# Performance work log

Measured on AMD Instinct MI355X. Metric: run time of the kernel, lower is better.

## Reference

```python
import jax, jax.numpy as jnp
import numpy as np

N_NODES = 50000
N_EDGES = 800000
HID = 256
HEADS = 4
HEAD_C = HID // HEADS  # 64
IN_CH = 16
OUT_CH = 4
NEG_SLOPE = 0.2  # PyG GATConv default LeakyReLU slope
LN_EPS = 1e-5


def setup_inputs() -> dict:
    key = jax.random.key(0)
    ks = jax.random.split(key, 12)
    s = 0.05
    return {
        "x": jax.random.normal(ks[0], (N_NODES, IN_CH), dtype=jnp.float32),
        "edge_index": jax.random.randint(ks[1], (2, N_EDGES), 0, N_NODES, dtype=jnp.int64),
        "w_in": jax.random.normal(ks[2], (IN_CH, HID), dtype=jnp.float32) * s,
        "b_in": jnp.zeros((HID,), dtype=jnp.float32),
        "w_gat": jax.random.normal(ks[3], (4, HID, HID), dtype=jnp.float32) * s,
        "att_src": jax.random.normal(ks[4], (4, HEADS, HEAD_C), dtype=jnp.float32) * s,
        "att_dst": jax.random.normal(ks[5], (4, HEADS, HEAD_C), dtype=jnp.float32) * s,
        "b_gat": jnp.zeros((4, HID), dtype=jnp.float32),
        "ln_scale": jnp.ones((4, HID), dtype=jnp.float32),
        "ln_bias": jnp.zeros((4, HID), dtype=jnp.float32),
        "w_out": jax.random.normal(ks[6], (HID, OUT_CH), dtype=jnp.float32) * s,
        "b_out": jnp.zeros((OUT_CH,), dtype=jnp.float32),
    }


def _gat_layer(x, src, dst, W, a_src, a_dst, bias, g, beta):
    """One GATConv(concat, heads=4) + LayerNorm + ELU. x:[N,HID]."""
    n = x.shape[0]
    h = (x @ W).reshape(n, HEADS, HEAD_C)                 # [N,H,C]
    a_s = jnp.einsum("nhc,hc->nh", h, a_src)              # [N,H]
    a_d = jnp.einsum("nhc,hc->nh", h, a_dst)              # [N,H]
    logits = jax.nn.leaky_relu(a_s[src] + a_d[dst], NEG_SLOPE)  # [E,H]
    # segment softmax over destination neighborhoods (self-loops ensure non-empty)
    m = jax.ops.segment_max(logits, dst, num_segments=n)
    e = jnp.exp(logits - m[dst])
    denom = jax.ops.segment_sum(e, dst, num_segments=n)
    alpha = e / (denom[dst] + 1e-16)                      # [E,H]
    msg = alpha[:, :, None] * h[src]                      # [E,H,C]
    out = jax.ops.segment_sum(msg, dst, num_segments=n).reshape(n, HID) + bias
    mu = out.mean(-1, keepdims=True)
    var = out.var(-1, keepdims=True)
    out = (out - mu) * jax.lax.rsqrt(var + LN_EPS) * g + beta
    return jax.nn.elu(out)


def reference(x, edge_index, w_in, b_in, w_gat, att_src, att_dst, b_gat,
              ln_scale, ln_bias, w_out, b_out):
    n = x.shape[0]
    # PyG GATConv adds self-loops by default
    loops = jnp.arange(n, dtype=edge_index.dtype)
    ei = jnp.concatenate([edge_index, jnp.stack([loops, loops])], axis=1)
    src, dst = ei[0], ei[1]

    x = x @ w_in + b_in                                   # input_proj
    h = x
    for l in (0, 1):
        h = _gat_layer(h, src, dst, w_gat[l], att_src[l], att_dst[l],
                       b_gat[l], ln_scale[l], ln_bias[l])
    x = x + h
    h = x
    for l in (2, 3):
        h = _gat_layer(h, src, dst, w_gat[l], att_src[l], att_dst[l],
                       b_gat[l], ln_scale[l], ln_bias[l])
    x = x + h
    return x @ w_out + b_out
```

## Files before the change

kernel.cpp:

```cpp
#include <hip/hip_runtime.h>
#include <math.h>

#define NN 50000
#define E0 800000
#define ET 850000
#define HID 256
#define INCH 16
#define MAXDEG 64

typedef _Float16 h8 __attribute__((ext_vector_type(8)));
typedef float f32x4 __attribute__((ext_vector_type(4)));

__global__ void scatter_pad_kernel(const int* __restrict__ ei, int* __restrict__ cursor,
                                   int* __restrict__ csr_pad) {
    int e = blockIdx.x * blockDim.x + threadIdx.x;
    if (e >= ET) return;
    int s, d;
    if (e < E0) { s = ei[e]; d = ei[E0 + e]; }
    else        { s = d = e - E0; }
    int pos = atomicAdd(&cursor[d], 1);
    if (pos < MAXDEG) csr_pad[(d << 6) + pos] = s;
}

__global__ __launch_bounds__(256) void wt_kernel(const float* __restrict__ w,
                                                 _Float16* __restrict__ wt) {
    int k = blockIdx.x, l = blockIdx.y, n = threadIdx.x;
    float v = w[((size_t)l * 256 + k) * 256 + n];
    wt[((size_t)l * 256 + n) * 256 + k] = (_Float16)v;
}

__global__ __launch_bounds__(256) void input_proj_kernel(
    const float* __restrict__ x, const float* __restrict__ w,
    const float* __restrict__ b, _Float16* __restrict__ outh) {
    int n = blockIdx.x, j = threadIdx.x;
    __shared__ float xs[INCH];
    if (j < INCH) xs[j] = x[n * INCH + j];
    __syncthreads();
    float acc = b[j];
#pragma unroll
    for (int k = 0; k < INCH; k++) acc += xs[k] * w[k * HID + j];
    outh[n * HID + j] = (_Float16)acc;
}

__global__ __launch_bounds__(512) void gemm_fused_kernel(
    const _Float16* __restrict__ A, const _Float16* __restrict__ BT,
    _Float16* __restrict__ H, const float* __restrict__ att_s,
    const float* __restrict__ att_d, float* __restrict__ AS, float* __restrict__ AD,
    int N) {
    int t = threadIdx.x;
    int wv = t >> 6, lane = t & 63;
    int rb = blockIdx.x * 128;
    int wr = (wv >> 2) * 64, wc = (wv & 3) * 64;
    int lm = lane & 15, lq = lane >> 4;
    f32x4 acc[4][4] = {};

    const _Float16* ap[4];
#pragma unroll
    for (int i = 0; i < 4; ++i) {
        int ra = rb + wr + i * 16 + lm;
        if (ra >= N) ra = N - 1;
        ap[i] = A + (size_t)ra * 256 + lq * 8;
    }
    const _Float16* bp[4];
#pragma unroll
    for (int j = 0; j < 4; ++j)
        bp[j] = BT + (size_t)(wc + j * 16 + lm) * 256 + lq * 8;

#pragma unroll 2
    for (int k0 = 0; k0 < 256; k0 += 32) {
        h8 af[4], bfr[4];
#pragma unroll
        for (int i = 0; i < 4; ++i) af[i] = *(const h8*)(ap[i] + k0);
#pragma unroll
        for (int j = 0; j < 4; ++j) bfr[j] = *(const h8*)(bp[j] + k0);
#pragma unroll
        for (int i = 0; i < 4; ++i)
#pragma unroll
            for (int j = 0; j < 4; ++j)
                acc[i][j] = __builtin_amdgcn_mfma_f32_16x16x32_f16(af[i], bfr[j], acc[i][j], 0, 0, 0);
    }

    int head = wv & 3;
    float sa[4], sd[4];
#pragma unroll
    for (int j = 0; j < 4; ++j) {
        sa[j] = att_s[head * 64 + j * 16 + lm];
        sd[j] = att_d[head * 64 + j * 16 + lm];
    }
#pragma unroll
    for (int i = 0; i < 4; ++i)
#pragma unroll
        for (int rr = 0; rr < 4; ++rr) {
            float vs = acc[i][0][rr] * sa[0] + acc[i][1][rr] * sa[1]
                     + acc[i][2][rr] * sa[2] + acc[i][3][rr] * sa[3];
            float vd = acc[i][0][rr] * sd[0] + acc[i][1][rr] * sd[1]
                     + acc[i][2][rr] * sd[2] + acc[i][3][rr] * sd[3];
#pragma unroll
            for (int o = 1; o <= 8; o <<= 1) {
                vs += __shfl_xor(vs, o, 64);
                vd += __shfl_xor(vd, o, 64);
            }
            int row = rb + wr + i * 16 + lq * 4 + rr;
            if (lm == 0 && row < N) {
                AS[row * 4 + head] = vs;
                AD[row * 4 + head] = vd;
            }
        }

#pragma unroll
    for (int i = 0; i < 4; ++i)
#pragma unroll
        for (int j = 0; j < 4; ++j) {
            int col = wc + j * 16 + lm;
#pragma unroll
            for (int rr = 0; rr < 4; ++rr) {
                int row = rb + wr + i * 16 + lq * 4 + rr;
                if (row < N) H[(size_t)row * 256 + col] = (_Float16)acc[i][j][rr];
            }
        }
}

__global__ __launch_bounds__(256) void agg_kernel(
    const _Float16* __restrict__ H, const float4* __restrict__ AS,
    const float4* __restrict__ AD,
    const int* __restrict__ cnt, const int* __restrict__ csr_pad,
    const float* __restrict__ bias, const float* __restrict__ g, const float* __restrict__ beta,
    const _Float16* __restrict__ res, _Float16* __restrict__ outh) {
    int t = threadIdx.x;
    int l32 = t & 31;
    int n = blockIdx.x * 8 + (t >> 5);
    int deg = cnt[n];
    if (deg > MAXDEG) deg = MAXDEG;
    int start = n << 6, end = start + deg;
    float4 adv = AD[n];
    int head = l32 >> 3;
    int c0 = l32 * 8;
    float advh = (head == 0) ? adv.x : (head == 1) ? adv.y : (head == 2) ? adv.z : adv.w;

    float acc[8] = {};
    float acc_e = 0.f;
#pragma unroll 4
    for (int i = start; i < end; ++i) {
        int s = csr_pad[i];
        const float* as = (const float*)&AS[s];
        float v = as[head] + advh;
        v = (v >= 0.f) ? v : 0.2f * v;
        float e = __expf(v);
        acc_e += e;
        h8 hv = *(const h8*)(H + (size_t)s * 256 + c0);
#pragma unroll
        for (int k = 0; k < 8; ++k) acc[k] += e * (float)hv[k];
    }
    float dinv = 1.f / (acc_e + 1e-16f);

    float val[8];
#pragma unroll
    for (int k = 0; k < 8; k += 4) {
        float4 bb = *(const float4*)(bias + c0 + k);
        val[k]     = acc[k]     * dinv + bb.x;
        val[k + 1] = acc[k + 1] * dinv + bb.y;
        val[k + 2] = acc[k + 2] * dinv + bb.z;
        val[k + 3] = acc[k + 3] * dinv + bb.w;
    }

    float s1 = 0.f, s2 = 0.f;
#pragma unroll
    for (int k = 0; k < 8; ++k) { s1 += val[k]; s2 += val[k] * val[k]; }
#pragma unroll
    for (int o = 16; o >= 1; o >>= 1) {
        s1 += __shfl_xor(s1, o, 64);
        s2 += __shfl_xor(s2, o, 64);
    }
    float mu = s1 * (1.f / 256.f);
    float var = s2 * (1.f / 256.f) - mu * mu;
    float rs = rsqrtf(var + 1e-5f);

    float y[8];
#pragma unroll
    for (int k = 0; k < 8; k += 4) {
        float4 g4 = *(const float4*)(g + c0 + k);
        float4 b4 = *(const float4*)(beta + c0 + k);
        y[k]     = (val[k]     - mu) * rs * g4.x + b4.x;
        y[k + 1] = (val[k + 1] - mu) * rs * g4.y + b4.y;
        y[k + 2] = (val[k + 2] - mu) * rs * g4.z + b4.z;
        y[k + 3] = (val[k + 3] - mu) * rs * g4.w + b4.w;
    }
#pragma unroll
    for (int k = 0; k < 8; ++k) y[k] = (y[k] > 0.f) ? y[k] : (__expf(y[k]) - 1.f);
    if (res) {
        h8 r0 = *(const h8*)(res + (size_t)n * 256 + c0);
#pragma unroll
        for (int k = 0; k < 8; ++k) y[k] += (float)r0[k];
    }
    h8 o0;
#pragma unroll
    for (int k = 0; k < 8; ++k) o0[k] = (_Float16)y[k];
    *(h8*)(outh + (size_t)n * 256 + c0) = o0;
}

__global__ __launch_bounds__(256) void out_proj_kernel(
    const _Float16* __restrict__ x, const float* __restrict__ w,
    const float* __restrict__ b, float* __restrict__ out, int n) {
    int tid = blockIdx.x * blockDim.x + threadIdx.x;
    int node = tid >> 6, lane = tid & 63;
    if (node >= n) return;
    const _Float16* xp = x + (size_t)node * HID + lane * 4;
    float x0 = (float)xp[0], x1 = (float)xp[1], x2 = (float)xp[2], x3 = (float)xp[3];
    const float4* wr = (const float4*)w;
    float4 w0 = wr[lane * 4 + 0];
    float4 w1 = wr[lane * 4 + 1];
    float4 w2 = wr[lane * 4 + 2];
    float4 w3 = wr[lane * 4 + 3];
    float o0 = x0 * w0.x + x1 * w1.x + x2 * w2.x + x3 * w3.x;
    float o1 = x0 * w0.y + x1 * w1.y + x2 * w2.y + x3 * w3.y;
    float o2 = x0 * w0.z + x1 * w1.z + x2 * w2.z + x3 * w3.z;
    float o3 = x0 * w0.w + x1 * w1.w + x2 * w2.w + x3 * w3.w;
#pragma unroll
    for (int o = 32; o >= 1; o >>= 1) {
        o0 += __shfl_down(o0, o, 64);
        o1 += __shfl_down(o1, o, 64);
        o2 += __shfl_down(o2, o, 64);
        o3 += __shfl_down(o3, o, 64);
    }
    if (lane == 0) {
        out[node * 4 + 0] = o0 + b[0];
        out[node * 4 + 1] = o1 + b[1];
        out[node * 4 + 2] = o2 + b[2];
        out[node * 4 + 3] = o3 + b[3];
    }
}

extern "C" void kernel_launch(void* const* d_in, const int* in_sizes, int n_in,
                              void* d_out, int out_size, void* d_ws, size_t ws_size,
                              hipStream_t stream) {
    const float* x       = (const float*)d_in[0];
    const int*   ei      = (const int*)  d_in[1];
    const float* w_in    = (const float*)d_in[2];
    const float* b_in    = (const float*)d_in[3];
    const float* w_gat   = (const float*)d_in[4];
    const float* att_src = (const float*)d_in[5];
    const float* att_dst = (const float*)d_in[6];
    const float* b_gat   = (const float*)d_in[7];
    const float* ln_g    = (const float*)d_in[8];
    const float* ln_b    = (const float*)d_in[9];
    const float* w_out   = (const float*)d_in[10];
    const float* b_out   = (const float*)d_in[11];
    float* out = (float*)d_out;

    char* ws = (char*)d_ws;
    size_t off = 0;
    auto alloc = [&](size_t bytes) {
        void* p = ws + off;
        off += (bytes + 255) & ~(size_t)255;
        return p;
    };
    _Float16*  Ph      = (_Float16*)alloc((size_t)NN * HID * 2);
    _Float16*  Ch      = (_Float16*)alloc((size_t)NN * HID * 2);
    _Float16*  Gh      = (_Float16*)alloc((size_t)NN * HID * 2);
    _Float16*  H       = (_Float16*)alloc((size_t)NN * HID * 2);
    _Float16*  WT      = (_Float16*)alloc((size_t)4 * HID * HID * 2);
    float*     ASAD    = (float*)alloc((size_t)NN * 8 * 4);
    int*       cursor  = (int*)alloc((size_t)NN * 4);
    int*       csr_pad = (int*)alloc((size_t)NN * MAXDEG * 4);

    float* AS = ASAD;
    float* AD = ASAD + (size_t)NN * 4;

    const int NB_EDGE = (ET + 255) / 256;
    const int NB_GEMM = (NN + 127) / 128;
    const int NB_AGG = NN / 8;

    hipMemsetAsync(cursor, 0, (size_t)NN * 4, stream);
    scatter_pad_kernel<<<NB_EDGE, 256, 0, stream>>>(ei, cursor, csr_pad);

    wt_kernel<<<dim3(256, 4), 256, 0, stream>>>(w_gat, WT);
    input_proj_kernel<<<NN, 256, 0, stream>>>(x, w_in, b_in, Ph);

    auto run_layer = [&](const _Float16* inh, int l, const _Float16* res, _Float16* outh) {
        gemm_fused_kernel<<<NB_GEMM, 512, 0, stream>>>(
            inh, WT + (size_t)l * HID * HID, H,
            att_src + l * 256, att_dst + l * 256, AS, AD, NN);
        agg_kernel<<<NB_AGG, 256, 0, stream>>>(
            H, (const float4*)AS, (const float4*)AD, cursor, csr_pad,
            b_gat + l * 256, ln_g + l * 256, ln_b + l * 256, res, outh);
    };

    run_layer(Ph, 0, nullptr, Gh);
    run_layer(Gh, 1, Ph,      Ch);
    run_layer(Ch, 2, nullptr, Gh);
    run_layer(Gh, 3, Ch,      Ph);

    out_proj_kernel<<<(NN * 64 + 255) / 256, 256, 0, stream>>>(Ph, w_out, b_out, out, NN);
}
```

Before: 616.1 us.

## Fuse all stages into one persistent cooperative kernel with grid syncs

```diff
diff --git a/kernel.cpp b/kernel.cpp
--- a/kernel.cpp
+++ b/kernel.cpp
@@ -1,5 +1,8 @@
 #include <hip/hip_runtime.h>
+#include <hip/hip_cooperative_groups.h>
 #include <math.h>
+
+namespace cg = cooperative_groups;
 
 #define NN 50000
 #define E0 800000
@@ -7,246 +10,268 @@
 #define HID 256
 #define INCH 16
 #define MAXDEG 64
-
+#define NT64 782
+#define NGRP (NN / 8)
+
+typedef _Float16 h4 __attribute__((ext_vector_type(4)));
 typedef _Float16 h8 __attribute__((ext_vector_type(8)));
 typedef float f32x4 __attribute__((ext_vector_type(4)));
 
-__global__ void scatter_pad_kernel(const int* __restrict__ ei, int* __restrict__ cursor,
-                                   int* __restrict__ csr_pad) {
-    int e = blockIdx.x * blockDim.x + threadIdx.x;
-    if (e >= ET) return;
-    int s, d;
-    if (e < E0) { s = ei[e]; d = ei[E0 + e]; }
-    else        { s = d = e - E0; }
-    int pos = atomicAdd(&cursor[d], 1);
-    if (pos < MAXDEG) csr_pad[(d << 6) + pos] = s;
-}
-
-__global__ __launch_bounds__(256) void wt_kernel(const float* __restrict__ w,
-                                                 _Float16* __restrict__ wt) {
-    int k = blockIdx.x, l = blockIdx.y, n = threadIdx.x;
-    float v = w[((size_t)l * 256 + k) * 256 + n];
-    wt[((size_t)l * 256 + n) * 256 + k] = (_Float16)v;
-}
-
-__global__ __launch_bounds__(256) void input_proj_kernel(
-    const float* __restrict__ x, const float* __restrict__ w,
-    const float* __restrict__ b, _Float16* __restrict__ outh) {
-    int n = blockIdx.x, j = threadIdx.x;
-    __shared__ float xs[INCH];
-    if (j < INCH) xs[j] = x[n * INCH + j];
-    __syncthreads();
-    float acc = b[j];
-#pragma unroll
-    for (int k = 0; k < INCH; k++) acc += xs[k] * w[k * HID + j];
-    outh[n * HID + j] = (_Float16)acc;
-}
-
-__global__ __launch_bounds__(512) void gemm_fused_kernel(
+struct KParams {
+    const float* x; const int* ei;
+    const float* w_in; const float* b_in;
+    const float* w_gat; const float* att_src; const float* att_dst;
+    const float* b_gat; const float* ln_g; const float* ln_b;
+    const float* w_out; const float* b_out;
+    float* out;
+    _Float16* Ph; _Float16* Ch; _Float16* Gh; _Float16* H; _Float16* WT;
+    float* AS; float* AD;
+    int* cursor; int* csr_pad; int* tickets;
+};
+
+__device__ __forceinline__ void gemm_phase(
     const _Float16* __restrict__ A, const _Float16* __restrict__ BT,
     _Float16* __restrict__ H, const float* __restrict__ att_s,
-    const float* __restrict__ att_d, float* __restrict__ AS, float* __restrict__ AD,
-    int N) {
+    const float* __restrict__ att_d, float* __restrict__ AS, float* __restrict__ AD) {
     int t = threadIdx.x;
     int wv = t >> 6, lane = t & 63;
-    int rb = blockIdx.x * 128;
-    int wr = (wv >> 2) * 64, wc = (wv & 3) * 64;
+    int wc = wv * 64;
     int lm = lane & 15, lq = lane >> 4;
-    f32x4 acc[4][4] = {};
-
-    const _Float16* ap[4];
-#pragma unroll
-    for (int i = 0; i < 4; ++i) {
-        int ra = rb + wr + i * 16 + lm;
-        if (ra >= N) ra = N - 1;
-        ap[i] = A + (size_t)ra * 256 + lq * 8;
-    }
+
     const _Float16* bp[4];
 #pragma unroll
     for (int j = 0; j < 4; ++j)
         bp[j] = BT + (size_t)(wc + j * 16 + lm) * 256 + lq * 8;
 
+    float sa[4], sd[4];
+#pragma unroll
+    for (int j = 0; j < 4; ++j) {
+        sa[j] = att_s[wv * 64 + j * 16 + lm];
+        sd[j] = att_d[wv * 64 + j * 16 + lm];
+    }
+
+    for (int tile = blockIdx.x; tile < NT64; tile += gridDim.x) {
+        int rb = tile * 64;
+        f32x4 acc[4][4] = {};
+        const _Float16* ap[4];
+#pragma unroll
+        for (int i = 0; i < 4; ++i) {
+            int ra = rb + i * 16 + lm;
+            if (ra >= NN) ra = NN - 1;
+            ap[i] = A + (size_t)ra * 256 + lq * 8;
+        }
 #pragma unroll 2
-    for (int k0 = 0; k0 < 256; k0 += 32) {
-        h8 af[4], bfr[4];
-#pragma unroll
-        for (int i = 0; i < 4; ++i) af[i] = *(const h8*)(ap[i] + k0);
-#pragma unroll
-        for (int j = 0; j < 4; ++j) bfr[j] = *(const h8*)(bp[j] + k0);
+        for (int k0 = 0; k0 < 256; k0 += 32) {
+            h8 af[4], bfr[4];
+#pragma unroll
+            for (int i = 0; i < 4; ++i) af[i] = *(const h8*)(ap[i] + k0);
+#pragma unroll
+            for (int j = 0; j < 4; ++j) bfr[j] = *(const h8*)(bp[j] + k0);
+#pragma unroll
+            for (int i = 0; i < 4; ++i)
+#pragma unroll
+                for (int j = 0; j < 4; ++j)
+                    acc[i][j] = __builtin_amdgcn_mfma_f32_16x16x32_f16(af[i], bfr[j], acc[i][j], 0, 0, 0);
+        }
 #pragma unroll
         for (int i = 0; i < 4; ++i)
 #pragma unroll
-            for (int j = 0; j < 4; ++j)
-                acc[i][j] = __builtin_amdgcn_mfma_f32_16x16x32_f16(af[i], bfr[j], acc[i][j], 0, 0, 0);
-    }
-
-    int head = wv & 3;
-    float sa[4], sd[4];
-#pragma unroll
-    for (int j = 0; j < 4; ++j) {
-        sa[j] = att_s[head * 64 + j * 16 + lm];
-        sd[j] = att_d[head * 64 + j * 16 + lm];
-    }
-#pragma unroll
-    for (int i = 0; i < 4; ++i)
-#pragma unroll
-        for (int rr = 0; rr < 4; ++rr) {
-            float vs = acc[i][0][rr] * sa[0] + acc[i][1][rr] * sa[1]
-                     + acc[i][2][rr] * sa[2] + acc[i][3][rr] * sa[3];
-            float vd = acc[i][0][rr] * sd[0] + acc[i][1][rr] * sd[1]
-                     + acc[i][2][rr] * sd[2] + acc[i][3][rr] * sd[3];
-#pragma unroll
-            for (int o = 1; o <= 8; o <<= 1) {
-                vs += __shfl_xor(vs, o, 64);
-                vd += __shfl_xor(vd, o, 64);
+            for (int rr = 0; rr < 4; ++rr) {
+                float vs = acc[i][0][rr] * sa[0] + acc[i][1][rr] * sa[1]
+                         + acc[i][2][rr] * sa[2] + acc[i][3][rr] * sa[3];
+                float vd = acc[i][0][rr] * sd[0] + acc[i][1][rr] * sd[1]
+                         + acc[i][2][rr] * sd[2] + acc[i][3][rr] * sd[3];
+#pragma unroll
+                for (int o = 1; o <= 8; o <<= 1) {
+                    vs += __shfl_xor(vs, o, 64);
+                    vd += __shfl_xor(vd, o, 64);
+                }
+                int row = rb + i * 16 + lq * 4 + rr;
+                if (lm == 0 && row < NN) {
+                    AS[row * 4 + wv] = vs;
+                    AD[row * 4 + wv] = vd;
+                }
             }
-            int row = rb + wr + i * 16 + lq * 4 + rr;
-            if (lm == 0 && row < N) {
-                AS[row * 4 + head] = vs;
-                AD[row * 4 + head] = vd;
+#pragma unroll
+        for (int i = 0; i < 4; ++i)
+#pragma unroll
+            for (int j = 0; j < 4; ++j) {
+                int col = wc + j * 16 + lm;
+#pragma unroll
+                for (int rr = 0; rr < 4; ++rr) {
+                    int row = rb + i * 16 + lq * 4 + rr;
+                    if (row < NN) H[(size_t)row * 256 + col] = (_Float16)acc[i][j][rr];
+                }
             }
-        }
-
-#pragma unroll
-    for (int i = 0; i < 4; ++i)
-#pragma unroll
-        for (int j = 0; j < 4; ++j) {
-            int col = wc + j * 16 + lm;
-#pragma unroll
-            for (int rr = 0; rr < 4; ++rr) {
-                int row = rb + wr + i * 16 + lq * 4 + rr;
-                if (row < N) H[(size_t)row * 256 + col] = (_Float16)acc[i][j][rr];
-            }
-        }
+    }
 }
 
-__global__ __launch_bounds__(256) void agg_kernel(
-    const _Float16* __restrict__ H, const float4* __restrict__ AS,
-    const float4* __restrict__ AD,
+__device__ __forceinline__ void agg_phase(
+    const _Float16* __restrict__ H, const float4* __restrict__ AS4,
+    const float4* __restrict__ AD4,
     const int* __restrict__ cnt, const int* __restrict__ csr_pad,
-    const float* __restrict__ bias, const float* __restrict__ g, const float* __restrict__ beta,
-    const _Float16* __restrict__ res, _Float16* __restrict__ outh) {
+    const float* __restrict__ bias, const float* __restrict__ g,
+    const float* __restrict__ beta,
+    const _Float16* __restrict__ res, _Float16* __restrict__ outh, int* ctr) {
     int t = threadIdx.x;
     int l32 = t & 31;
-    int n = blockIdx.x * 8 + (t >> 5);
-    int deg = cnt[n];
-    if (deg > MAXDEG) deg = MAXDEG;
-    int start = n << 6, end = start + deg;
-    float4 adv = AD[n];
+    int sub = t >> 5;
     int head = l32 >> 3;
     int c0 = l32 * 8;
-    float advh = (head == 0) ? adv.x : (head == 1) ? adv.y : (head == 2) ? adv.z : adv.w;
-
-    float acc[8] = {};
-    float acc_e = 0.f;
+    __shared__ int sg;
+    for (;;) {
+        __syncthreads();
+        if (t == 0) sg = atomicAdd(ctr, 1);
+        __syncthreads();
+        int grp = sg;
+        if (grp >= NGRP) break;
+        int n = grp * 8 + sub;
+        int deg = cnt[n];
+        if (deg > MAXDEG) deg = MAXDEG;
+        int start = n << 6, end = start + deg;
+        float4 adv = AD4[n];
+        float advh = (head == 0) ? adv.x : (head == 1) ? adv.y : (head == 2) ? adv.z : adv.w;
+
+        float acc[8] = {};
+        float acc_e = 0.f;
 #pragma unroll 4
-    for (int i = start; i < end; ++i) {
-        int s = csr_pad[i];
-        const float* as = (const float*)&AS[s];
-        float v = as[head] + advh;
-        v = (v >= 0.f) ? v : 0.2f * v;
-        float e = __expf(v);
-        acc_e += e;
-        h8 hv = *(const h8*)(H + (size_t)s * 256 + c0);
-#pragma unroll
-        for (int k = 0; k < 8; ++k) acc[k] += e * (float)hv[k];
-    }
-    float dinv = 1.f / (acc_e + 1e-16f);
-
-    float val[8];
-#pragma unroll
-    for (int k = 0; k < 8; k += 4) {
-        float4 bb = *(const float4*)(bias + c0 + k);
-        val[k]     = acc[k]     * dinv + bb.x;
-        val[k + 1] = acc[k + 1] * dinv + bb.y;
-        val[k + 2] = acc[k + 2] * dinv + bb.z;
-        val[k + 3] = acc[k + 3] * dinv + bb.w;
-    }
-
-    float s1 = 0.f, s2 = 0.f;
-#pragma unroll
-    for (int k = 0; k < 8; ++k) { s1 += val[k]; s2 += val[k] * val[k]; }
-#pragma unroll
-    for (int o = 16; o >= 1; o >>= 1) {
-        s1 += __shfl_xor(s1, o, 64);
-        s2 += __shfl_xor(s2, o, 64);
-    }
-    float mu = s1 * (1.f / 256.f);
-    float var = s2 * (1.f / 256.f) - mu * mu;
-    float rs = rsqrtf(var + 1e-5f);
-
-    float y[8];
-#pragma unroll
-    for (int k = 0; k < 8; k += 4) {
-        float4 g4 = *(const float4*)(g + c0 + k);
-        float4 b4 = *(const float4*)(beta + c0 + k);
-        y[k]     = (val[k]     - mu) * rs * g4.x + b4.x;
-        y[k + 1] = (val[k + 1] - mu) * rs * g4.y + b4.y;
-        y[k + 2] = (val[k + 2] - mu) * rs * g4.z + b4.z;
-        y[k + 3] = (val[k + 3] - mu) * rs * g4.w + b4.w;
-    }
-#pragma unroll
-    for (int k = 0; k < 8; ++k) y[k] = (y[k] > 0.f) ? y[k] : (__expf(y[k]) - 1.f);
-    if (res) {
-        h8 r0 = *(const h8*)(res + (size_t)n * 256 + c0);
-#pragma unroll
-        for (int k = 0; k < 8; ++k) y[k] += (float)r0[k];
-    }
-    h8 o0;
-#pragma unroll
-    for (int k = 0; k < 8; ++k) o0[k] = (_Float16)y[k];
-    *(h8*)(outh + (size_t)n * 256 + c0) = o0;
+        for (int i = start; i < end; ++i) {
+            int s = csr_pad[i];
+            const float* as = (const float*)&AS4[s];
+            float v = as[head] + advh;
+            v = (v >= 0.f) ? v : 0.2f * v;
+            float e = __expf(v);
+            acc_e += e;
+            h8 hv = *(const h8*)(H + (size_t)s * 256 + c0);
+#pragma unroll
+            for (int k = 0; k < 8; ++k) acc[k] += e * (float)hv[k];
+        }
+        float dinv = 1.f / (acc_e + 1e-16f);
+
+        float val[8];
+#pragma unroll
+        for (int k = 0; k < 8; k += 4) {
+            float4 bb = *(const float4*)(bias + c0 + k);
+            val[k]     = acc[k]     * dinv + bb.x;
+            val[k + 1] = acc[k + 1] * dinv + bb.y;
+            val[k + 2] = acc[k + 2] * dinv + bb.z;
+            val[k + 3] = acc[k + 3] * dinv + bb.w;
+        }
+        float s1 = 0.f, s2 = 0.f;
+#pragma unroll
+        for (int k = 0; k < 8; ++k) { s1 += val[k]; s2 += val[k] * val[k]; }
+#pragma unroll
+        for (int o = 16; o >= 1; o >>= 1) {
+            s1 += __shfl_xor(s1, o, 64);
+            s2 += __shfl_xor(s2, o, 64);
+        }
+        float mu = s1 * (1.f / 256.f);
+        float var = s2 * (1.f / 256.f) - mu * mu;
+        float rs = rsqrtf(var + 1e-5f);
+
+        float y[8];
+#pragma unroll
+        for (int k = 0; k < 8; k += 4) {
+            float4 g4 = *(const float4*)(g + c0 + k);
+            float4 b4 = *(const float4*)(beta + c0 + k);
+            y[k]     = (val[k]     - mu) * rs * g4.x + b4.x;
+            y[k + 1] = (val[k + 1] - mu) * rs * g4.y + b4.y;
+            y[k + 2] = (val[k + 2] - mu) * rs * g4.z + b4.z;
+            y[k + 3] = (val[k + 3] - mu) * rs * g4.w + b4.w;
+        }
+#pragma unroll
+        for (int k = 0; k < 8; ++k) y[k] = (y[k] > 0.f) ? y[k] : (__expf(y[k]) - 1.f);
+        if (res) {
+            h8 r0 = *(const h8*)(res + (size_t)n * 256 + c0);
+#pragma unroll
+            for (int k = 0; k < 8; ++k) y[k] += (float)r0[k];
+        }
+        h8 o0;
+#pragma unroll
+        for (int k = 0; k < 8; ++k) o0[k] = (_Float16)y[k];
+        *(h8*)(outh + (size_t)n * 256 + c0) = o0;
+    }
 }
 
-__global__ __launch_bounds__(256) void out_proj_kernel(
-    const _Float16* __restrict__ x, const float* __restrict__ w,
-    const float* __restrict__ b, float* __restrict__ out, int n) {
-    int tid = blockIdx.x * blockDim.x + threadIdx.x;
-    int node = tid >> 6, lane = tid & 63;
-    if (node >= n) return;
-    const _Float16* xp = x + (size_t)node * HID + lane * 4;
-    float x0 = (float)xp[0], x1 = (float)xp[1], x2 = (float)xp[2], x3 = (float)xp[3];
-    const float4* wr = (const float4*)w;
-    float4 w0 = wr[lane * 4 + 0];
-    float4 w1 = wr[lane * 4 + 1];
-    float4 w2 = wr[lane * 4 + 2];
-    float4 w3 = wr[lane * 4 + 3];
-    float o0 = x0 * w0.x + x1 * w1.x + x2 * w2.x + x3 * w3.x;
-    float o1 = x0 * w0.y + x1 * w1.y + x2 * w2.y + x3 * w3.y;
-    float o2 = x0 * w0.z + x1 * w1.z + x2 * w2.z + x3 * w3.z;
-    float o3 = x0 * w0.w + x1 * w1.w + x2 * w2.w + x3 * w3.w;
-#pragma unroll
-    for (int o = 32; o >= 1; o >>= 1) {
-        o0 += __shfl_down(o0, o, 64);
-        o1 += __shfl_down(o1, o, 64);
-        o2 += __shfl_down(o2, o, 64);
-        o3 += __shfl_down(o3, o, 64);
-    }
-    if (lane == 0) {
-        out[node * 4 + 0] = o0 + b[0];
-        out[node * 4 + 1] = o1 + b[1];
-        out[node * 4 + 2] = o2 + b[2];
-        out[node * 4 + 3] = o3 + b[3];
+__global__ __launch_bounds__(256, 4) void mega_kernel(KParams p) {
+    cg::grid_group grid = cg::this_grid();
+    int t = threadIdx.x;
+    int gsize = gridDim.x * blockDim.x;
+    int gtid = blockIdx.x * blockDim.x + t;
+
+    for (int e = gtid; e < ET; e += gsize) {
+        int s, d;
+        if (e < E0) { s = p.ei[e]; d = p.ei[E0 + e]; }
+        else        { s = d = e - E0; }
+        int pos = atomicAdd(&p.cursor[d], 1);
+        if (pos < MAXDEG) p.csr_pad[(d << 6) + pos] = s;
+    }
+    for (int idx = gtid; idx < 4 * 256 * 256; idx += gsize) {
+        int l = idx >> 16, rem = idx & 65535, k = rem >> 8, n = rem & 255;
+        p.WT[((size_t)l * 256 + n) * 256 + k] = (_Float16)p.w_gat[idx];
+    }
+    for (int idx = gtid; idx < NN * 64; idx += gsize) {
+        int n = idx >> 6, c0 = (idx & 63) * 4;
+        const float* xr = p.x + n * INCH;
+        float4 a = *(const float4*)(p.b_in + c0);
+#pragma unroll
+        for (int k = 0; k < INCH; ++k) {
+            float xv = xr[k];
+            const float4 wv4 = *(const float4*)(p.w_in + k * 256 + c0);
+            a.x += xv * wv4.x; a.y += xv * wv4.y; a.z += xv * wv4.z; a.w += xv * wv4.w;
+        }
+        h4 o = { (_Float16)a.x, (_Float16)a.y, (_Float16)a.z, (_Float16)a.w };
+        *(h4*)(p.Ph + (size_t)n * 256 + c0) = o;
+    }
+    grid.sync();
+
+    const _Float16* ins[4]  = { p.Ph, p.Gh, p.Ch, p.Gh };
+    const _Float16* ress[4] = { nullptr, p.Ph, nullptr, p.Ch };
+    _Float16*       outs[4] = { p.Gh, p.Ch, p.Gh, p.Ph };
+
+    for (int l = 0; l < 4; ++l) {
+        gemm_phase(ins[l], p.WT + (size_t)l * 65536, p.H,
+                   p.att_src + l * 256, p.att_dst + l * 256, p.AS, p.AD);
+        grid.sync();
+        agg_phase(p.H, (const float4*)p.AS, (const float4*)p.AD,
+                  p.cursor, p.csr_pad,
+                  p.b_gat + l * 256, p.ln_g + l * 256, p.ln_b + l * 256,
+                  ress[l], outs[l], &p.tickets[l]);
+        grid.sync();
+    }
+
+    for (int idx = gtid; idx < NN * 64; idx += gsize) {
+        int node = idx >> 6, lane = idx & 63;
+        const _Float16* xp = p.Ph + (size_t)node * HID + lane * 4;
+        float x0 = (float)xp[0], x1 = (float)xp[1], x2 = (float)xp[2], x3 = (float)xp[3];
+        const float4* wr = (const float4*)p.w_out;
+        float4 w0 = wr[lane * 4 + 0];
+        float4 w1 = wr[lane * 4 + 1];
+        float4 w2 = wr[lane * 4 + 2];
+        float4 w3 = wr[lane * 4 + 3];
+        float o0 = x0 * w0.x + x1 * w1.x + x2 * w2.x + x3 * w3.x;
+        float o1 = x0 * w0.y + x1 * w1.y + x2 * w2.y + x3 * w3.y;
+        float o2 = x0 * w0.z + x1 * w1.z + x2 * w2.z + x3 * w3.z;
+        float o3 = x0 * w0.w + x1 * w1.w + x2 * w2.w + x3 * w3.w;
+#pragma unroll
+        for (int o = 32; o >= 1; o >>= 1) {
+            o0 += __shfl_down(o0, o, 64);
+            o1 += __shfl_down(o1, o, 64);
+            o2 += __shfl_down(o2, o, 64);
+            o3 += __shfl_down(o3, o, 64);
+        }
+        if (lane == 0) {
+            p.out[node * 4 + 0] = o0 + p.b_out[0];
+            p.out[node * 4 + 1] = o1 + p.b_out[1];
+            p.out[node * 4 + 2] = o2 + p.b_out[2];
+            p.out[node * 4 + 3] = o3 + p.b_out[3];
+        }
     }
 }
 
 extern "C" void kernel_launch(void* const* d_in, const int* in_sizes, int n_in,
                               void* d_out, int out_size, void* d_ws, size_t ws_size,
                               hipStream_t stream) {
-    const float* x       = (const float*)d_in[0];
-    const int*   ei      = (const int*)  d_in[1];
-    const float* w_in    = (const float*)d_in[2];
-    const float* b_in    = (const float*)d_in[3];
-    const float* w_gat   = (const float*)d_in[4];
-    const float* att_src = (const float*)d_in[5];
-    const float* att_dst = (const float*)d_in[6];
-    const float* b_gat   = (const float*)d_in[7];
-    const float* ln_g    = (const float*)d_in[8];
-    const float* ln_b    = (const float*)d_in[9];
-    const float* w_out   = (const float*)d_in[10];
-    const float* b_out   = (const float*)d_in[11];
-    float* out = (float*)d_out;
-
     char* ws = (char*)d_ws;
     size_t off = 0;
     auto alloc = [&](size_t bytes) {
@@ -254,41 +279,41 @@
         off += (bytes + 255) & ~(size_t)255;
         return p;
     };
-    _Float16*  Ph      = (_Float16*)alloc((size_t)NN * HID * 2);
-    _Float16*  Ch      = (_Float16*)alloc((size_t)NN * HID * 2);
-    _Float16*  Gh      = (_Float16*)alloc((size_t)NN * HID * 2);
-    _Float16*  H       = (_Float16*)alloc((size_t)NN * HID * 2);
-    _Float16*  WT      = (_Float16*)alloc((size_t)4 * HID * HID * 2);
-    float*     ASAD    = (float*)alloc((size_t)NN * 8 * 4);
-    int*       cursor  = (int*)alloc((size_t)NN * 4);
-    int*       csr_pad = (int*)alloc((size_t)NN * MAXDEG * 4);
-
-    float* AS = ASAD;
-    float* AD = ASAD + (size_t)NN * 4;
-
-    const int NB_EDGE = (ET + 255) / 256;
-    const int NB_GEMM = (NN + 127) / 128;
-    const int NB_AGG = NN / 8;
-
-    hipMemsetAsync(cursor, 0, (size_t)NN * 4, stream);
-    scatter_pad_kernel<<<NB_EDGE, 256, 0, stream>>>(ei, cursor, csr_pad);
-
-    wt_kernel<<<dim3(256, 4), 256, 0, stream>>>(w_gat, WT);
-    input_proj_kernel<<<NN, 256, 0, stream>>>(x, w_in, b_in, Ph);
-
-    auto run_layer = [&](const _Float16* inh, int l, const _Float16* res, _Float16* outh) {
-        gemm_fused_kernel<<<NB_GEMM, 512, 0, stream>>>(
-            inh, WT + (size_t)l * HID * HID, H,
-            att_src + l * 256, att_dst + l * 256, AS, AD, NN);
-        agg_kernel<<<NB_AGG, 256, 0, stream>>>(
-            H, (const float4*)AS, (const float4*)AD, cursor, csr_pad,
-            b_gat + l * 256, ln_g + l * 256, ln_b + l * 256, res, outh);
-    };
-
-    run_layer(Ph, 0, nullptr, Gh);
-    run_layer(Gh, 1, Ph,      Ch);
-    run_layer(Ch, 2, nullptr, Gh);
-    run_layer(Gh, 3, Ch,      Ph);
-
-    out_proj_kernel<<<(NN * 64 + 255) / 256, 256, 0, stream>>>(Ph, w_out, b_out, out, NN);
+    _Float16* Ph      = (_Float16*)alloc((size_t)NN * HID * 2);
+    _Float16* Ch      = (_Float16*)alloc((size_t)NN * HID * 2);
+    _Float16* Gh      = (_Float16*)alloc((size_t)NN * HID * 2);
+    _Float16* H       = (_Float16*)alloc((size_t)NN * HID * 2);
+    _Float16* WT      = (_Float16*)alloc((size_t)4 * HID * HID * 2);
+    float*    ASAD    = (float*)alloc((size_t)NN * 8 * 4);
+    int*      cursor  = (int*)alloc((size_t)(NN + 16) * 4);
+    int*      csr_pad = (int*)alloc((size_t)NN * MAXDEG * 4);
+    int*      tickets = cursor + NN;
+
+    KParams prm;
+    prm.x       = (const float*)d_in[0];
+    prm.ei      = (const int*)  d_in[1];
+    prm.w_in    = (const float*)d_in[2];
+    prm.b_in    = (const float*)d_in[3];
+    prm.w_gat   = (const float*)d_in[4];
+    prm.att_src = (const float*)d_in[5];
+    prm.att_dst = (const float*)d_in[6];
+    prm.b_gat   = (const float*)d_in[7];
+    prm.ln_g    = (const float*)d_in[8];
+    prm.ln_b    = (const float*)d_in[9];
+    prm.w_out   = (const float*)d_in[10];
+    prm.b_out   = (const float*)d_in[11];
+    prm.out     = (float*)d_out;
+    prm.Ph = Ph; prm.Ch = Ch; prm.Gh = Gh; prm.H = H; prm.WT = WT;
+    prm.AS = ASAD; prm.AD = ASAD + (size_t)NN * 4;
+    prm.cursor = cursor; prm.csr_pad = csr_pad; prm.tickets = tickets;
+
+    hipMemsetAsync(cursor, 0, (size_t)(NN + 16) * 4, stream);
+
+    int maxb = 0;
+    hipOccupancyMaxActiveBlocksPerMultiprocessor(&maxb, mega_kernel, 256, 0);
+    if (maxb < 1) maxb = 1;
+    if (maxb > 8) maxb = 8;
+    dim3 grid(256 * maxb), block(256);
+    void* args[] = { (void*)&prm };
+    hipLaunchCooperativeKernel(mega_kernel, grid, block, args, 0, stream);
 }
```

Result: slower. 1.420 ms (+130.5%).
